# Kernel tuning notes

Measured on AMD Instinct MI355X. Metric: run time of the kernel, lower is better.

Reference implementation:

```python
import jax, jax.numpy as jnp
import numpy as np

EPS_LOG = 1e-12  # clamp for BCE logs (torch clamps log at -100)


def _gather_feat(feat, ind):
    # feat: [B, C, Hf, Wf] -> gather at flat spatial index ind [B, K] -> [B, K, C]
    B, C, Hf, Wf = feat.shape
    flat = feat.reshape(B, C, Hf * Wf).transpose(0, 2, 1)  # [B, Hf*Wf, C]
    return jnp.take_along_axis(flat, ind[:, :, None], axis=1)  # [B, K, C]


def setup_inputs() -> dict:
    key = jax.random.key(0)
    ks = jax.random.split(key, 6)
    B, K, N, Hf, Wf, H, W = 2, 64, 16, 128, 128, 128, 128
    centers = jax.random.normal(ks[0], (B, 2 * N, Hf, Wf), dtype=jnp.float32)
    radius = jax.random.uniform(ks[1], (B, 1, Hf, Wf), dtype=jnp.float32) * 5.0 + 1.0
    mask = jax.random.uniform(ks[2], (B, K), dtype=jnp.float32)
    ind = jax.random.randint(ks[3], (B, K), 0, Hf * Wf).astype(jnp.int64)
    target = jax.random.uniform(ks[4], (B, K, H, W), dtype=jnp.float32)
    peak = jax.random.uniform(ks[5], (B, K, 2), dtype=jnp.float32) * W
    return {"centers": centers, "radius": radius, "mask": mask, "ind": ind,
            "target": target, "peak": peak}


def reference(centers, radius, mask, ind, target, peak):
    B, C, Hf, Wf = centers.shape
    K = ind.shape[1]
    N = C // 2
    H, W = target.shape[2], target.shape[3]

    pred = _gather_feat(centers, ind)                 # [B, K, 2N]
    pred_radius = _gather_feat(radius, ind)[..., 0]   # [B, K]

    # even channels = x (matched against column index), odd = y (row index)
    pred = pred.reshape(B, K, N, 2) + peak[:, :, None, :]  # [B, K, N, 2]

    # grid[h, w] = (w, h), matching torch's [[ [i, j] for i in range(W)] for j in range(H)]
    gx, gy = jnp.meshgrid(jnp.arange(W, dtype=jnp.float32),
                          jnp.arange(H, dtype=jnp.float32))  # each [H, W]
    grid = jnp.stack([gx, gy], axis=-1)  # [H, W, 2]

    diff = pred[:, :, None, None, :, :] - grid[None, None, :, :, None, :]  # [B,K,H,W,N,2]
    neg_sq = -jnp.sum(diff * diff, axis=-1)                                # [B,K,H,W,N]
    denom = 2.0 * (pred_radius ** 2)[:, :, None, None, None]               # [B,K,1,1,1]
    g = jnp.sum(jnp.exp(neg_sq / denom), axis=-1)                          # [B,K,H,W]
    pred_map = jax.nn.sigmoid(g)  # ceiling == 'sigmoid'

    m = mask[:, :, None, None]  # broadcast over [H, W]
    p = pred_map * m
    t = target * m
    # BCELoss(reduction='mean')
    bce = -(t * jnp.log(jnp.clip(p, EPS_LOG, 1.0)) +
            (1.0 - t) * jnp.log(jnp.clip(1.0 - p, EPS_LOG, 1.0)))
    loss = jnp.mean(bce)
    return (loss, loss)
```

## Files before the change

kernel.cpp:

```cpp
#include <hip/hip_runtime.h>
#include <hip/hip_bf16.h>

#define B_ 2
#define K_ 64
#define N_ 16
#define C_ 32
#define HF_ 128
#define WF_ 128
#define H_ 128
#define W_ 128
#define HW_ (H_ * W_)
#define TILES_PER_BK (HW_ / 256)
#define NBLOCKS (B_ * K_ * TILES_PER_BK)
#define TOTAL_ELEMS ((double)(B_ * K_ * H_ * W_))

__global__ __launch_bounds__(256) void gauss_bce_partial(
    const float* __restrict__ centers,
    const float* __restrict__ radius,
    const float* __restrict__ mask,
    const int*   __restrict__ ind,
    const float* __restrict__ target,
    const float* __restrict__ peak,
    float* __restrict__ partials)
{
    __shared__ float sx[N_];
    __shared__ float sy[N_];
    __shared__ float s_inv2r2;
    __shared__ float s_m;
    __shared__ float warp_sums[4];

    const int tid  = threadIdx.x;
    const int bk   = blockIdx.x >> 6;
    const int tile = blockIdx.x & 63;
    const int b = bk >> 6;
    const int k = bk & 63;

    if (tid < C_) {
        const int ii = ind[b * K_ + k];
        const float v = centers[(size_t)(b * C_ + tid) * (HF_ * WF_) + ii];
        const int n = tid >> 1;
        if ((tid & 1) == 0) {
            sx[n] = v + peak[(b * K_ + k) * 2 + 0];
        } else {
            sy[n] = v + peak[(b * K_ + k) * 2 + 1];
        }
    } else if (tid == C_) {
        const int ii = ind[b * K_ + k];
        const float r = radius[(size_t)b * (HF_ * WF_) + ii];
        s_inv2r2 = 1.0f / (2.0f * r * r);
    } else if (tid == C_ + 1) {
        s_m = mask[b * K_ + k];
    }
    __syncthreads();

    const int pix = tile * 256 + tid;
    const int h = pix >> 7;
    const int w = pix & 127;
    const float fx = (float)w;
    const float fy = (float)h;
    const float inv2r2 = s_inv2r2;
    const float m = s_m;

    float g = 0.0f;
    #pragma unroll
    for (int n = 0; n < N_; ++n) {
        const float dx = sx[n] - fx;
        const float dy = sy[n] - fy;
        g += __expf(-(dx * dx + dy * dy) * inv2r2);
    }

    const float sig = 1.0f / (1.0f + __expf(-g));
    float p = sig * m;
    const float t = target[((size_t)(b * K_ + k) * H_ + h) * W_ + w] * m;

    float pc  = fminf(fmaxf(p, 1e-12f), 1.0f);
    float omp = fminf(fmaxf(1.0f - p, 1e-12f), 1.0f);
    float bce = -(t * __logf(pc) + (1.0f - t) * __logf(omp));

    float v = bce;
    #pragma unroll
    for (int off = 32; off > 0; off >>= 1)
        v += __shfl_down(v, off, 64);
    const int lane = tid & 63;
    const int wid  = tid >> 6;
    if (lane == 0) warp_sums[wid] = v;
    __syncthreads();
    if (tid == 0) {
        partials[blockIdx.x] = warp_sums[0] + warp_sums[1] + warp_sums[2] + warp_sums[3];
    }
}

__global__ __launch_bounds__(256) void reduce_final(
    const float* __restrict__ partials, float* __restrict__ out)
{
    __shared__ double warp_sums[4];
    const int tid = threadIdx.x;
    double acc = 0.0;
    #pragma unroll
    for (int i = 0; i < NBLOCKS / 256; ++i)
        acc += (double)partials[i * 256 + tid];

    #pragma unroll
    for (int off = 32; off > 0; off >>= 1)
        acc += __shfl_down(acc, off, 64);
    const int lane = tid & 63;
    const int wid  = tid >> 6;
    if (lane == 0) warp_sums[wid] = acc;
    __syncthreads();
    if (tid == 0) {
        double s = warp_sums[0] + warp_sums[1] + warp_sums[2] + warp_sums[3];
        float loss = (float)(s / TOTAL_ELEMS);
        out[0] = loss;
        out[1] = loss;
    }
}

extern "C" void kernel_launch(void* const* d_in, const int* in_sizes, int n_in,
                              void* d_out, int out_size, void* d_ws, size_t ws_size,
                              hipStream_t stream) {
    const float* centers = (const float*)d_in[0];
    const float* radius  = (const float*)d_in[1];
    const float* mask    = (const float*)d_in[2];
    const int*   ind     = (const int*)d_in[3];
    const float* target  = (const float*)d_in[4];
    const float* peak    = (const float*)d_in[5];
    float* out = (float*)d_out;
    float* partials = (float*)d_ws;

    gauss_bce_partial<<<NBLOCKS, 256, 0, stream>>>(
        centers, radius, mask, ind, target, peak, partials);
    reduce_final<<<1, 256, 0, stream>>>(partials, out);
}
```

Baseline: 82.66 us.

## Process four pixels per thread with float4 target loads and exp2 folding

Each thread now handles four consecutive pixels in a row, so grid size drops by four. The per-row dy^2 terms and the Gaussian centres are hoisted into registers and reused across all four pixels. Target is read with one float4 load per thread. The -log2(e)/(2r^2) constant is folded so each term is a single FMA plus exp2, and the sigmoid uses a hardware reciprocal. This cuts block setup, LDS traffic and per-exp arithmetic, at the cost of more registers per thread and fewer blocks to hide latency.

```diff
diff --git a/kernel.cpp b/kernel.cpp
--- a/kernel.cpp
+++ b/kernel.cpp
@@ -10,9 +10,12 @@
 #define H_ 128
 #define W_ 128
 #define HW_ (H_ * W_)
-#define TILES_PER_BK (HW_ / 256)
+#define PIX_PER_THREAD 4
+#define PIX_PER_BLOCK (256 * PIX_PER_THREAD)
+#define TILES_PER_BK (HW_ / PIX_PER_BLOCK)
 #define NBLOCKS (B_ * K_ * TILES_PER_BK)
 #define TOTAL_ELEMS ((double)(B_ * K_ * H_ * W_))
+#define LOG2E 1.44269504088896f
 
 __global__ __launch_bounds__(256) void gauss_bce_partial(
     const float* __restrict__ centers,
@@ -25,13 +28,13 @@
 {
     __shared__ float sx[N_];
     __shared__ float sy[N_];
-    __shared__ float s_inv2r2;
+    __shared__ float s_c2;
     __shared__ float s_m;
     __shared__ float warp_sums[4];
 
     const int tid  = threadIdx.x;
-    const int bk   = blockIdx.x >> 6;
-    const int tile = blockIdx.x & 63;
+    const int bk   = blockIdx.x >> 4;
+    const int tile = blockIdx.x & (TILES_PER_BK - 1);
     const int b = bk >> 6;
     const int k = bk & 63;
 
@@ -47,37 +50,50 @@
     } else if (tid == C_) {
         const int ii = ind[b * K_ + k];
         const float r = radius[(size_t)b * (HF_ * WF_) + ii];
-        s_inv2r2 = 1.0f / (2.0f * r * r);
+        s_c2 = -LOG2E / (2.0f * r * r);
     } else if (tid == C_ + 1) {
         s_m = mask[b * K_ + k];
     }
     __syncthreads();
 
-    const int pix = tile * 256 + tid;
-    const int h = pix >> 7;
-    const int w = pix & 127;
-    const float fx = (float)w;
+    const int pix0 = tile * PIX_PER_BLOCK + tid * PIX_PER_THREAD;
+    const int h  = pix0 >> 7;
+    const int w0 = pix0 & 127;
     const float fy = (float)h;
-    const float inv2r2 = s_inv2r2;
-    const float m = s_m;
+    const float c2 = s_c2;
+    const float m  = s_m;
 
-    float g = 0.0f;
+    const float4 t4 = *(const float4*)&target[((size_t)(b * K_ + k) * H_ + h) * W_ + w0];
+    const float tvals[4] = {t4.x, t4.y, t4.z, t4.w};
+
+    float dy2[N_], sxr[N_];
     #pragma unroll
     for (int n = 0; n < N_; ++n) {
-        const float dx = sx[n] - fx;
         const float dy = sy[n] - fy;
-        g += __expf(-(dx * dx + dy * dy) * inv2r2);
+        dy2[n] = dy * dy;
+        sxr[n] = sx[n];
     }
 
-    const float sig = 1.0f / (1.0f + __expf(-g));
-    float p = sig * m;
-    const float t = target[((size_t)(b * K_ + k) * H_ + h) * W_ + w] * m;
+    float acc = 0.0f;
+    #pragma unroll
+    for (int j = 0; j < PIX_PER_THREAD; ++j) {
+        const float fx = (float)(w0 + j);
+        float g = 0.0f;
+        #pragma unroll
+        for (int n = 0; n < N_; ++n) {
+            const float dx = sxr[n] - fx;
+            g += exp2f(__builtin_fmaf(dx, dx, dy2[n]) * c2);
+        }
+        const float e   = __expf(-g);
+        const float sig = __builtin_amdgcn_rcpf(1.0f + e);
+        const float p = sig * m;
+        const float t = tvals[j] * m;
+        const float pc  = fminf(fmaxf(p, 1e-12f), 1.0f);
+        const float omp = fminf(fmaxf(1.0f - p, 1e-12f), 1.0f);
+        acc += -(t * __logf(pc) + (1.0f - t) * __logf(omp));
+    }
 
-    float pc  = fminf(fmaxf(p, 1e-12f), 1.0f);
-    float omp = fminf(fmaxf(1.0f - p, 1e-12f), 1.0f);
-    float bce = -(t * __logf(pc) + (1.0f - t) * __logf(omp));
-
-    float v = bce;
+    float v = acc;
     #pragma unroll
     for (int off = 32; off > 0; off >>= 1)
         v += __shfl_down(v, off, 64);
```

Result: no change. 82.62 us (-0.0%).
